# Optimization experiments

Measured on AMD Instinct MI355X. Metric: run time of the kernel, lower is better.

Reference implementation:

```python
import jax, jax.numpy as jnp
from jax import lax
import numpy as np

DN = ('NCDHW', 'OIDHW', 'NCDHW')
EPS = 1e-3  # BatchNorm1d eps=0.001
GRID = (41, 512, 512)  # spatial_shape [40,512,512] + [1,0,0]


def _block(x, mask, w, gamma, beta, rmean, rvar, stride, padding):
    # Regular (non-submanifold) sparse conv computes the same values as a dense
    # conv on the zero-filled grid; active OUTPUT sites are exactly those reached
    # by any active input site through the kernel window. BN+ReLU act only on
    # active sites (inactive sites stay exactly 0), hence the mask multiply.
    y = lax.conv_general_dilated(x, w, stride, padding, dimension_numbers=DN)
    k1 = jnp.ones((1, 1) + w.shape[2:], x.dtype)
    m = lax.conv_general_dilated(mask, k1, stride, padding, dimension_numbers=DN)
    m = (m > 0).astype(x.dtype)
    inv = gamma / jnp.sqrt(rvar + EPS)
    scale = inv.reshape(1, -1, 1, 1, 1)
    shift = (beta - rmean * inv).reshape(1, -1, 1, 1, 1)
    return jax.nn.relu(y * scale + shift) * m, m


def setup_inputs() -> dict:
    key = jax.random.key(0)
    NV, B = 120000, 2
    kf, kb, kz, ky, kx, kp = jax.random.split(key, 6)
    voxel_features = jax.random.normal(kf, (NV, 3), jnp.float32)
    coors = jnp.stack([
        jax.random.randint(kb, (NV,), 0, B, jnp.int32),
        jax.random.randint(kz, (NV,), 0, 40, jnp.int32),
        jax.random.randint(ky, (NV,), 0, 512, jnp.int32),
        jax.random.randint(kx, (NV,), 0, 512, jnp.int32)], axis=1)
    inp = {"voxel_features": voxel_features, "coors": coors, "batch_size": B}
    chans = [(3, 16, (3, 3, 3)), (16, 32, (3, 3, 3)), (32, 64, (3, 3, 3)), (64, 64, (3, 1, 1))]
    for i, (ci, co, k) in enumerate(chans, 1):
        kw, kg, kbb, km, kv = jax.random.split(jax.random.fold_in(kp, i), 5)
        fan = ci * k[0] * k[1] * k[2]
        inp[f"w{i}"] = jax.random.normal(kw, (co, ci) + k, jnp.float32) / np.sqrt(fan).astype(np.float32)
        inp[f"g{i}"] = jax.random.uniform(kg, (co,), jnp.float32, 0.5, 1.5)
        inp[f"bb{i}"] = jax.random.normal(kbb, (co,), jnp.float32) * 0.1
        inp[f"rm{i}"] = jax.random.normal(km, (co,), jnp.float32) * 0.1
        inp[f"rv{i}"] = jax.random.uniform(kv, (co,), jnp.float32, 0.5, 1.5)
    return inp


def reference(voxel_features, coors, batch_size,
              w1, g1, bb1, rm1, rv1,
              w2, g2, bb2, rm2, rv2,
              w3, g3, bb3, rm3, rv3,
              w4, g4, bb4, rm4, rv4):
    D, H, W = GRID
    C = voxel_features.shape[1]
    b, z, y, x = coors[:, 0], coors[:, 1], coors[:, 2], coors[:, 3]
    dense = jnp.zeros((batch_size, C, D, H, W), voxel_features.dtype)
    dense = dense.at[b, :, z, y, x].add(voxel_features)  # scatter voxels to grid
    mask = jnp.zeros((batch_size, 1, D, H, W), voxel_features.dtype).at[b, 0, z, y, x].set(1.0)
    h, m = _block(dense, mask, w1, g1, bb1, rm1, rv1, (2, 2, 2), [(1, 1), (1, 1), (1, 1)])
    h, m = _block(h, m, w2, g2, bb2, rm2, rv2, (2, 2, 2), [(1, 1), (1, 1), (1, 1)])
    h, m = _block(h, m, w3, g3, bb3, rm3, rv3, (2, 2, 2), [(0, 0), (1, 1), (1, 1)])
    h, m = _block(h, m, w4, g4, bb4, rm4, rv4, (2, 1, 1), [(0, 0), (0, 0), (0, 0)])
    N, Co, Dd, Hh, Ww = h.shape  # [B, 64, 2, 64, 64]
    return h.reshape(N, Co * Dd, Hh, Ww)
```

## Files before the change

kernel.cpp:

```cpp
#include <hip/hip_runtime.h>

#define EPS 1e-3f


static __device__ __forceinline__ unsigned f2bf(float f) {
    unsigned u = __float_as_uint(f);
    return (u + 0x7FFFu + ((u >> 16) & 1u)) >> 16;
}

typedef _Float16 f16x8 __attribute__((ext_vector_type(8)));
typedef float f32x4 __attribute__((ext_vector_type(4)));
typedef float f32x16 __attribute__((ext_vector_type(16)));

#define Y1_BYTES   88080384
#define SLACK_BYTE 2752512
#define SLACK_Y1   90832912

__global__ __launch_bounds__(256) void repack_prezero(
    const float* __restrict__ g1, const float* __restrict__ b1,
    const float* __restrict__ rm1, const float* __restrict__ rv1,
    const float* __restrict__ w2, const float* __restrict__ g2, const float* __restrict__ b2,
    const float* __restrict__ rm2, const float* __restrict__ rv2,
    const float* __restrict__ w3, const float* __restrict__ g3, const float* __restrict__ b3,
    const float* __restrict__ rm3, const float* __restrict__ rv3,
    const float* __restrict__ w4, const float* __restrict__ g4, const float* __restrict__ b4,
    const float* __restrict__ rm4, const float* __restrict__ rv4,
    _Float16* __restrict__ wB2, _Float16* __restrict__ wB3,
    _Float16* __restrict__ wB4, float* __restrict__ shb,
    const int* __restrict__ coors, int NV, unsigned short* __restrict__ y1,
    unsigned char* __restrict__ m1, float* __restrict__ m3)
{
    if (blockIdx.x >= 1034) {
        const int i = (blockIdx.x - 1034) * 256 + threadIdx.x;
        if (i < NV) {
            const int b = coors[4 * i + 0];
            const int z = coors[4 * i + 1];
            const int y = coors[4 * i + 2];
            const int x = coors[4 * i + 3];
            int ozv[2], nz = 0, oyv[2], ny = 0, oxv[2], nx = 0;
#pragma unroll
            for (int k = 0; k < 3; ++k) {
                int t = z + 1 - k;
                if (t >= 0 && !(t & 1)) { int o = t >> 1; if (o < 21) ozv[nz++] = o; }
            }
#pragma unroll
            for (int k = 0; k < 3; ++k) {
                int t = y + 1 - k;
                if (t >= 0 && !(t & 1)) { int o = t >> 1; if (o < 256) oyv[ny++] = o; }
            }
#pragma unroll
            for (int k = 0; k < 3; ++k) {
                int t = x + 1 - k;
                if (t >= 0 && !(t & 1)) { int o = t >> 1; if (o < 256) oxv[nx++] = o; }
            }
            const uint4 zz = {0u, 0u, 0u, 0u};
            for (int a = 0; a < nz; ++a)
                for (int bb = 0; bb < ny; ++bb)
                    for (int c = 0; c < nx; ++c) {
                        const int sp = ozv[a] * 65536 + oyv[bb] * 256 + oxv[c];
                        uint4* p = (uint4*)(y1 + (size_t)(b * 1376256 + sp) * 16);
                        p[0] = zz;
                        p[1] = zz;
                    }
        }
        asm volatile("s_waitcnt vmcnt(0)" ::: "memory");
        return;
    }
    if (blockIdx.x >= 321) {
        const int idx16 = (blockIdx.x - 321) * 256 + threadIdx.x;
        const uint4 zz = {0u, 0u, 0u, 0u};
        if (idx16 < 172034) {
            ((uint4*)m1)[idx16] = zz;
        } else if (idx16 < 182274) {
            ((uint4*)m3)[idx16 - 172034] = zz;
        }
        return;
    }

    const int i = blockIdx.x * 256 + threadIdx.x;
    if (i < 13824) {
        const int j = i & 7, lane = (i >> 3) & 63, tap = i >> 9;
        const int oc = lane & 31;
        const int cin = (lane >> 5) * 8 + j;
        const float inv = g2[oc] * rsqrtf(rv2[oc] + EPS);
        wB2[i] = (_Float16)(w2[(oc * 16 + cin) * 27 + tap] * inv);
    } else if (i >= 14336 && i < 69632) {
        const int j2 = i - 14336;
        const int j = j2 & 7, lane = (j2 >> 3) & 63, t = (j2 >> 9) & 3, tap = j2 >> 11;
        const int q = lane >> 4, n = lane & 15;
        const int oc = t * 16 + n;
        const int cin = q * 8 + j;
        const float inv = g3[oc] * rsqrtf(rv3[oc] + EPS);
        wB3[j2] = (_Float16)(w3[(oc * 32 + cin) * 27 + tap] * inv);
    } else if (i >= 69632 && i < 81920) {
        const int j2 = i - 69632;
        const int j = j2 & 7, lane = (j2 >> 3) & 63, t = (j2 >> 9) & 3, c = j2 >> 11;
        const int q = lane >> 4, n = lane & 15;
        const int oc = t * 16 + n;
        const int k = c * 32 + q * 8 + j;
        const int dz = k >> 6, cin = k & 63;
        const float inv = g4[oc] * rsqrtf(rv4[oc] + EPS);
        wB4[j2] = (_Float16)(w4[(oc * 64 + cin) * 3 + dz] * inv);
    } else if (i >= 81920 && i < 82112) {
        const int j = i - 81920;
        if (j < 32) {
            const float inv = g2[j] * rsqrtf(rv2[j] + EPS);
            shb[j] = b2[j] - rm2[j] * inv;
        } else if (j < 96) {
            const int o = j - 32;
            const float inv = g3[o] * rsqrtf(rv3[o] + EPS);
            shb[j] = b3[o] - rm3[o] * inv;
        } else if (j < 160) {
            const int o = j - 96;
            const float inv = g4[o] * rsqrtf(rv4[o] + EPS);
            shb[j] = b4[o] - rm4[o] * inv;
        } else if (j < 176) {
            const int o = j - 160;
            shb[j] = g1[o] * rsqrtf(rv1[o] + EPS);
        } else if (j < 192) {
            const int o = j - 176;
            const float inv = g1[o] * rsqrtf(rv1[o] + EPS);
            shb[j] = b1[o] - rm1[o] * inv;
        }
    }
}

__global__ __launch_bounds__(256) void scatter_l1(
    const float* __restrict__ vf, const int* __restrict__ coors, int NV,
    const float* __restrict__ w1, const float* __restrict__ shb,
    unsigned short* __restrict__ y1, unsigned char* __restrict__ m1)
{
    __shared__ float ws[16 * 3 * 27];
    for (int e = threadIdx.x; e < 16 * 3 * 27; e += 256)
        ws[e] = w1[e] * shb[160 + e / 81];
    __syncthreads();

    const int gid = blockIdx.x * 256 + threadIdx.x;
    const int i = gid >> 3;
    const int oc2 = gid & 7;
    if (i < NV) {
        const int oc = oc2 * 2;

        const int b = coors[4 * i + 0];
        const int z = coors[4 * i + 1];
        const int y = coors[4 * i + 2];
        const int x = coors[4 * i + 3];
        const float f0 = vf[3 * i + 0];
        const float f1 = vf[3 * i + 1];
        const float f2 = vf[3 * i + 2];

        int ozv[2], kzv[2], nz = 0;
        int oyv[2], kyv[2], ny = 0;
        int oxv[2], kxv[2], nx = 0;
#pragma unroll
        for (int k = 0; k < 3; ++k) {
            int t = z + 1 - k;
            if (t >= 0 && !(t & 1)) { int o = t >> 1; if (o < 21) { ozv[nz] = o; kzv[nz] = k; ++nz; } }
        }
#pragma unroll
        for (int k = 0; k < 3; ++k) {
            int t = y + 1 - k;
            if (t >= 0 && !(t & 1)) { int o = t >> 1; if (o < 256) { oyv[ny] = o; kyv[ny] = k; ++ny; } }
        }
#pragma unroll
        for (int k = 0; k < 3; ++k) {
            int t = x + 1 - k;
            if (t >= 0 && !(t & 1)) { int o = t >> 1; if (o < 256) { oxv[nx] = o; kxv[nx] = k; ++nx; } }
        }

        for (int a = 0; a < nz; ++a)
            for (int bb = 0; bb < ny; ++bb)
                for (int c = 0; c < nx; ++c) {
                    const int oz = ozv[a], oy = oyv[bb], ox = oxv[c];
                    const int tap = (kzv[a] * 3 + kyv[bb]) * 3 + kxv[c];
                    const int sp = oz * 65536 + oy * 256 + ox;
                    if (oc2 == 0) m1[b * 1376256 + sp] = 1;
                    const float s0 = ws[oc * 81 + tap] * f0 + ws[oc * 81 + 27 + tap] * f1 +
                                     ws[oc * 81 + 54 + tap] * f2;
                    const float s1 = ws[(oc + 1) * 81 + tap] * f0 +
                                     ws[(oc + 1) * 81 + 27 + tap] * f1 +
                                     ws[(oc + 1) * 81 + 54 + tap] * f2;
                    const unsigned pk = f2bf(s0) | (f2bf(s1) << 16);
                    unsigned* addr = (unsigned*)(y1 + (size_t)(b * 1376256 + sp) * 16 +
                                                 oc2 * 2);
                    asm volatile("global_atomic_pk_add_bf16 %0, %1, off"
                                 : : "v"(addr), "v"(pk) : "memory");
                }
    }
    asm volatile("s_waitcnt vmcnt(0)" ::: "memory");
}

__global__ __launch_bounds__(256) void masks_pass(
    const unsigned char* __restrict__ m1, float* __restrict__ m2,
    float* __restrict__ m3)
{
    const int idx = blockIdx.x * 256 + threadIdx.x;
    const int b = idx / 180224;
    const int r = idx - b * 180224;
    const int oz = r >> 14, r2 = r & 16383, oy = r2 >> 7, ox = r2 & 127;
    const int iz0 = 2 * oz - 1, iyb = 2 * oy - 1, ixb = 2 * ox - 1;
    unsigned msum = 0;
#pragma unroll
    for (int kz = 0; kz < 3; ++kz) {
        const int iz = iz0 + kz;
#pragma unroll
        for (int ky = 0; ky < 3; ++ky) {
            const int iy = iyb + ky;
#pragma unroll
            for (int kx = 0; kx < 3; ++kx) {
                const int ix = ixb + kx;
                if ((unsigned)iz < 21u && (unsigned)iy < 256u &&
                    (unsigned)ix < 256u)
                    msum |= m1[b * 1376256 + iz * 65536 + iy * 256 + ix];
            }
        }
    }
    m2[idx] = msum ? 1.f : 0.f;

    if (msum) {
        int ozv[2], nz = 0, oyv[2], ny = 0, oxv[2], nx = 0;
#pragma unroll
        for (int k = 0; k < 3; ++k) {
            int t = oz - k;
            if (t >= 0 && !(t & 1)) { int o = t >> 1; if (o < 5) ozv[nz++] = o; }
        }
#pragma unroll
        for (int k = 0; k < 3; ++k) {
            int t = oy + 1 - k;
            if (t >= 0 && !(t & 1)) { int o = t >> 1; if (o < 64) oyv[ny++] = o; }
        }
#pragma unroll
        for (int k = 0; k < 3; ++k) {
            int t = ox + 1 - k;
            if (t >= 0 && !(t & 1)) { int o = t >> 1; if (o < 64) oxv[nx++] = o; }
        }
        for (int a = 0; a < nz; ++a)
            for (int bb = 0; bb < ny; ++bb)
                for (int c = 0; c < nx; ++c)
                    m3[b * 20480 + ozv[a] * 4096 + oyv[bb] * 64 + oxv[c]] = 1.0f;
    }
}

__global__ __launch_bounds__(256) __attribute__((amdgpu_waves_per_eu(4, 8)))
void conv_l2(
    const unsigned char* __restrict__ y1c,
    const unsigned char* __restrict__ m1,
    const uint4* __restrict__ wB2,
    const float* __restrict__ m2, const float* __restrict__ shb,
    _Float16* __restrict__ h2h)
{
    const int tid = threadIdx.x;
    const int gw = blockIdx.x * 4 + (tid >> 6);
    const int lane = tid & 63;
    const int m = lane & 31, h = lane >> 5;

    const int plane = gw >> 9;
    const int rem = gw & 511;
    const int oy = rem >> 2;
    const int ox0 = (rem & 3) * 32;
    const int b = plane / 11, oz = plane % 11;
    const int iz0 = 2 * oz - 1, iyb = 2 * oy - 1;
    const int ixm = 2 * (ox0 + m) - 1;
    const int bbase = b * 1376256;
    const int qoff = h * 16;

    unsigned char mk[27];
#pragma unroll
    for (int t = 0; t < 27; ++t) {
        const int kz = t / 9, ky = (t / 3) % 3, kx = t % 3;
        const int iz = iz0 + kz, iy = iyb + ky, ix = ixm + kx;
        const bool v = (unsigned)iz < 21u && (unsigned)iy < 256u &&
                       (unsigned)ix < 256u;
        const int cell = bbase + iz * 65536 + iy * 256 + ix;
        mk[t] = m1[v ? cell : SLACK_BYTE];
    }

    float s1v[8];
    {
        const float4* sp = (const float4*)(shb + 176 + h * 8);
        const float4 a0 = sp[0], a1 = sp[1];
        s1v[0] = a0.x; s1v[1] = a0.y; s1v[2] = a0.z; s1v[3] = a0.w;
        s1v[4] = a1.x; s1v[5] = a1.y; s1v[6] = a1.z; s1v[7] = a1.w;
    }

    f32x16 acc;
#pragma unroll
    for (int r = 0; r < 16; ++r) acc[r] = 0.f;

    uint4 buf[13];
#pragma unroll
    for (int t = 0; t < 13; ++t) {
        const int kz = t / 9, ky = (t / 3) % 3, kx = t % 3;
        const int iz = iz0 + kz, iy = iyb + ky, ix = ixm + kx;
        const int cell = bbase + iz * 65536 + iy * 256 + ix;
        const int off = mk[t] ? (cell * 32 + qoff) : SLACK_Y1;
        buf[t] = *(const uint4*)(y1c + off);
    }

#pragma unroll
    for (int tap = 0; tap < 27; ++tap) {
        const int s = tap % 13;
        const uint4 ua = buf[s];
        const bool act = mk[s + (tap - s)] != 0;
        if (tap + 13 < 27) {
            const int t2 = tap + 13;
            const int kz = t2 / 9, ky = (t2 / 3) % 3, kx = t2 % 3;
            const int iz = iz0 + kz, iy = iyb + ky, ix = ixm + kx;
            const int cell = bbase + iz * 65536 + iy * 256 + ix;
            const int off = mk[t2] ? (cell * 32 + qoff) : SLACK_Y1;
            buf[s] = *(const uint4*)(y1c + off);
        }
        unsigned od[4];
        const unsigned dvs[4] = {ua.x, ua.y, ua.z, ua.w};
#pragma unroll
        for (int jj = 0; jj < 4; ++jj) {
            const unsigned dv = dvs[jj];
            const float vlo = fmaxf(__uint_as_float(dv << 16) + s1v[2 * jj], 0.f);
            const float vhi = fmaxf(__uint_as_float(dv & 0xFFFF0000u) + s1v[2 * jj + 1], 0.f);
            const unsigned pk =
                __builtin_bit_cast(unsigned, __builtin_amdgcn_cvt_pkrtz(vlo, vhi));
            od[jj] = act ? pk : 0u;
        }
        const uint4 uc = {od[0], od[1], od[2], od[3]};
        const f16x8 af = __builtin_bit_cast(f16x8, uc);
        const f16x8 bf = __builtin_bit_cast(f16x8, wB2[tap * 64 + lane]);
        acc = __builtin_amdgcn_mfma_f32_32x32x16_f16(af, bf, acc, 0, 0, 0);
    }

    const int oc = lane & 31;
#pragma unroll
    for (int r = 0; r < 16; ++r) {
        const int row = (r & 3) + 8 * (r >> 2) + 4 * h;
        const int px = ox0 + row;
        const int spo = oz * 16384 + oy * 128 + px;
        const float mv = m2[b * 180224 + spo];
        const size_t cbase = (size_t)(b * 180224 + spo) * 32;
        h2h[cbase + oc] = (_Float16)(fmaxf(acc[r] + shb[oc], 0.f) * mv);
    }
}

__global__ __launch_bounds__(256) __attribute__((amdgpu_waves_per_eu(4, 8)))
void conv_l3(
    const unsigned char* __restrict__ h2h,
    const uint4* __restrict__ wB3,
    const float* __restrict__ m3, const float* __restrict__ shb,
    _Float16* __restrict__ h3h)
{
    const int tid = threadIdx.x;
    const int gw = blockIdx.x * 4 + (tid >> 6);
    const int lane = tid & 63;
    const int m = lane & 15, q = lane >> 4;

    const int plane = gw >> 8;
    const int rem = gw & 255;
    const int oy = rem >> 2;
    const int ox0 = (rem & 3) * 16;
    const int b = plane / 5, oz = plane % 5;
    const int iz0 = 2 * oz, iyb = 2 * oy - 1;
    const int ixm = 2 * (ox0 + m) - 1;
    const int bbase = b * 180224;
    const int qoff = q * 16;

    f32x4 acc[4];
#pragma unroll
    for (int t = 0; t < 4; ++t) acc[t] = (f32x4){0.f, 0.f, 0.f, 0.f};

    uint4 buf[9];
    bool  val[9];
#pragma unroll
    for (int t = 0; t < 9; ++t) {
        const int ky = (t / 3) % 3, kx = t % 3;
        const int iz = iz0 + t / 9, iy = iyb + ky, ix = ixm + kx;
        const bool v = (unsigned)iy < 128u && (unsigned)ix < 128u;
        const int cell = bbase + iz * 16384 + iy * 128 + ix;
        buf[t] = *(const uint4*)(h2h + (v ? (cell * 64 + qoff) : 0));
        val[t] = v;
    }

#pragma unroll
    for (int tap = 0; tap < 27; ++tap) {
        const int s = tap % 9;
        uint4 ua = buf[s];
        if (!val[s]) { ua.x = 0; ua.y = 0; ua.z = 0; ua.w = 0; }
        if (tap + 9 < 27) {
            const int t2 = tap + 9;
            const int kz = t2 / 9, ky = (t2 / 3) % 3, kx = t2 % 3;
            const int iz = iz0 + kz, iy = iyb + ky, ix = ixm + kx;
            const bool v = (unsigned)iy < 128u && (unsigned)ix < 128u;
            const int cell = bbase + iz * 16384 + iy * 128 + ix;
            buf[s] = *(const uint4*)(h2h + (v ? (cell * 64 + qoff) : 0));
            val[s] = v;
        }
        const f16x8 af = __builtin_bit_cast(f16x8, ua);
#pragma unroll
        for (int t = 0; t < 4; ++t) {
            const f16x8 bf = __builtin_bit_cast(f16x8, wB3[(tap * 4 + t) * 64 + lane]);
            acc[t] = __builtin_amdgcn_mfma_f32_16x16x32_f16(af, bf, acc[t], 0, 0, 0);
        }
    }

    const int n = lane & 15;
#pragma unroll
    for (int r = 0; r < 4; ++r) {
        const int px = ox0 + q * 4 + r;
        const int spo = oz * 4096 + oy * 64 + px;
        const float mv = m3[b * 20480 + spo];
        const size_t cb = (size_t)(b * 20480 + spo) * 64;
#pragma unroll
        for (int t = 0; t < 4; ++t) {
            const int oc = t * 16 + n;
            h3h[cb + oc] = (_Float16)(fmaxf(acc[t][r] + shb[32 + oc], 0.f) * mv);
        }
    }
}

__global__ __launch_bounds__(256) __attribute__((amdgpu_waves_per_eu(4, 8)))
void conv_l4(
    const unsigned char* __restrict__ h3h,
    const uint4* __restrict__ wB4,
    const float* __restrict__ m3, const float* __restrict__ shb,
    float* __restrict__ out)
{
    const int tid = threadIdx.x;
    const int gw = blockIdx.x * 4 + (tid >> 6);
    const int lane = tid & 63;
    const int m = lane & 15, q = lane >> 4;

    const int b = gw >> 9, od = (gw >> 8) & 1;
    const int oy = (gw >> 2) & 63, ox0 = (gw & 3) * 16;
    const int cellbase = (b * 5 + 2 * od) * 4096 + oy * 64 + ox0 + m;

    f32x4 acc[4];
#pragma unroll
    for (int t = 0; t < 4; ++t) acc[t] = (f32x4){0.f, 0.f, 0.f, 0.f};

#pragma unroll
    for (int c = 0; c < 6; ++c) {
        const int dz = c >> 1;
        const size_t addr = (size_t)(cellbase + dz * 4096) * 128 +
                            (c & 1) * 64 + q * 16;
        const uint4 ua = *(const uint4*)(h3h + addr);
        const f16x8 af = __builtin_bit_cast(f16x8, ua);
#pragma unroll
        for (int t = 0; t < 4; ++t) {
            const f16x8 bf = __builtin_bit_cast(f16x8, wB4[(c * 4 + t) * 64 + lane]);
            acc[t] = __builtin_amdgcn_mfma_f32_16x16x32_f16(af, bf, acc[t], 0, 0, 0);
        }
    }

    const int n = lane & 15;
#pragma unroll
    for (int r = 0; r < 4; ++r) {
        const int px = ox0 + q * 4 + r;
        const int spo = oy * 64 + px;
        const float msum = m3[(b * 5 + 2 * od + 0) * 4096 + spo] +
                           m3[(b * 5 + 2 * od + 1) * 4096 + spo] +
                           m3[(b * 5 + 2 * od + 2) * 4096 + spo];
        const float mv = msum > 0.f ? 1.f : 0.f;
#pragma unroll
        for (int t = 0; t < 4; ++t) {
            const int oc = t * 16 + n;
            out[((b * 64 + oc) * 2 + od) * 4096 + spo] =
                fmaxf(acc[t][r] + shb[96 + oc], 0.f) * mv;
        }
    }
}

extern "C" void kernel_launch(void* const* d_in, const int* in_sizes, int n_in,
                              void* d_out, int out_size, void* d_ws, size_t ws_size,
                              hipStream_t stream)
{
    const float* vf    = (const float*)d_in[0];
    const int*   coors = (const int*)d_in[1];
    const float* w1 = (const float*)d_in[3];
    const float* g1 = (const float*)d_in[4];
    const float* b1 = (const float*)d_in[5];
    const float* rm1 = (const float*)d_in[6];
    const float* rv1 = (const float*)d_in[7];
    const float* w2 = (const float*)d_in[8];
    const float* g2 = (const float*)d_in[9];
    const float* b2 = (const float*)d_in[10];
    const float* rm2 = (const float*)d_in[11];
    const float* rv2 = (const float*)d_in[12];
    const float* w3 = (const float*)d_in[13];
    const float* g3 = (const float*)d_in[14];
    const float* b3 = (const float*)d_in[15];
    const float* rm3 = (const float*)d_in[16];
    const float* rv3 = (const float*)d_in[17];
    const float* w4 = (const float*)d_in[18];
    const float* g4 = (const float*)d_in[19];
    const float* b4 = (const float*)d_in[20];
    const float* rm4 = (const float*)d_in[21];
    const float* rv4 = (const float*)d_in[22];

    const int NV = in_sizes[0] / 3;

    float* ws = (float*)d_ws;
    float* y1  = ws;
    float* m1f = y1 + 22020096;
    float* h2h = m1f + 2752512;
    float* m2  = h2h + 5767168;
    float* h3h = m2 + 360448;
    float* m3  = h3h + 1310720;
    float* wB2 = m3 + 40960;
    float* wB3 = wB2 + 7168;
    float* wB4 = wB3 + 27648;
    float* shb = wB4 + 6144;

    unsigned char* m1 = (unsigned char*)m1f;

    const int pzBlocks = (NV + 255) / 256;
    repack_prezero<<<1034 + pzBlocks, 256, 0, stream>>>(
        g1, b1, rm1, rv1,
        w2, g2, b2, rm2, rv2, w3, g3, b3, rm3, rv3,
        w4, g4, b4, rm4, rv4,
        (_Float16*)wB2, (_Float16*)wB3, (_Float16*)wB4, shb,
        coors, NV, (unsigned short*)y1, m1, m3);
    scatter_l1<<<(NV * 8 + 255) / 256, 256, 0, stream>>>(vf, coors, NV, w1, shb,
                                                         (unsigned short*)y1, m1);
    masks_pass<<<1408, 256, 0, stream>>>(m1, m2, m3);
    conv_l2<<<2816, 256, 0, stream>>>((const unsigned char*)d_ws, m1,
                                      (const uint4*)wB2, m2, shb, (_Float16*)h2h);
    conv_l3<<<640, 256, 0, stream>>>((const unsigned char*)h2h, (const uint4*)wB3,
                                     m3, shb, (_Float16*)h3h);
    conv_l4<<<256, 256, 0, stream>>>((const unsigned char*)h3h, (const uint4*)wB4,
                                     m3, shb, (float*)d_out);
}
```

Measured before the change: 201.7 us.

## Stage conv_l2 input rows in LDS via global_load_lds with swizzle

The layer-2 conv kernel now has each block cover a full output row (4 waves × 32 x-positions). For each kz slice it cooperatively loads the three needed input rows into swizzled shared memory using direct global-to-LDS loads. Taps then read from LDS instead of issuing per-tap gathered global loads, so overlapping stride-2 windows reuse the same data and memory requests get more coalesced. Block indices are also remapped to interleave planes, and the per-tap mask is packed into a bitfield. The cost is added barriers per kz slice, no overlap between loading and compute, and 25 KB of LDS per block that may limit occupancy.

Measured after the change: 202.4 us. Within noise of the previous version (+0.4%).

```diff
diff --git a/kernel.cpp b/kernel.cpp
--- a/kernel.cpp
+++ b/kernel.cpp
@@ -12,7 +12,6 @@
 typedef float f32x4 __attribute__((ext_vector_type(4)));
 typedef float f32x16 __attribute__((ext_vector_type(16)));
 
-#define Y1_BYTES   88080384
 #define SLACK_BYTE 2752512
 #define SLACK_Y1   90832912
 
@@ -249,22 +248,25 @@
     const float* __restrict__ m2, const float* __restrict__ shb,
     _Float16* __restrict__ h2h)
 {
+    __shared__ unsigned char lds[3 * 8320];
+
     const int tid = threadIdx.x;
-    const int gw = blockIdx.x * 4 + (tid >> 6);
     const int lane = tid & 63;
+    const int w = tid >> 6;
     const int m = lane & 31, h = lane >> 5;
 
-    const int plane = gw >> 9;
-    const int rem = gw & 511;
-    const int oy = rem >> 2;
-    const int ox0 = (rem & 3) * 32;
-    const int b = plane / 11, oz = plane % 11;
+    const int sbid = (blockIdx.x & 7) * 352 + (blockIdx.x >> 3);
+    const int oy = sbid / 22;
+    const int plane = sbid - oy * 22;
+    const int b = plane / 11, oz = plane - b * 11;
+
+    const int ox0 = w * 32;
     const int iz0 = 2 * oz - 1, iyb = 2 * oy - 1;
     const int ixm = 2 * (ox0 + m) - 1;
     const int bbase = b * 1376256;
     const int qoff = h * 16;
 
-    unsigned char mk[27];
+    unsigned mbits = 0;
 #pragma unroll
     for (int t = 0; t < 27; ++t) {
         const int kz = t / 9, ky = (t / 3) % 3, kx = t % 3;
@@ -272,7 +274,7 @@
         const bool v = (unsigned)iz < 21u && (unsigned)iy < 256u &&
                        (unsigned)ix < 256u;
         const int cell = bbase + iz * 65536 + iy * 256 + ix;
-        mk[t] = m1[v ? cell : SLACK_BYTE];
+        mbits |= (unsigned)(m1[v ? cell : SLACK_BYTE] & 1) << t;
     }
 
     float s1v[8];
@@ -283,48 +285,81 @@
         s1v[4] = a1.x; s1v[5] = a1.y; s1v[6] = a1.z; s1v[7] = a1.w;
     }
 
+    int rdo[3];
+#pragma unroll
+    for (int kx = 0; kx < 3; ++kx) {
+        const unsigned lx = (unsigned)(2 * (ox0 + m) + kx);
+        const unsigned L = lx * 32 + qoff;
+        rdo[kx] = (int)(L ^ (((L >> 7) & 7u) << 4));
+    }
+
+    int su_row[7], su_ix[7], su_half[7];
+#pragma unroll
+    for (int it = 0; it < 7; ++it) {
+        const int t = it * 256 + tid;
+        const int row = t / 520;
+        const int u = t - row * 520;
+        const unsigned L = (unsigned)(u * 16) ^ (((unsigned)(u >> 3) & 7u) << 4);
+        su_row[it] = row;
+        su_ix[it] = (int)(L >> 5) - 1;
+        su_half[it] = (int)((L >> 4) & 1u);
+    }
+
     f32x16 acc;
 #pragma unroll
     for (int r = 0; r < 16; ++r) acc[r] = 0.f;
 
-    uint4 buf[13];
-#pragma unroll
-    for (int t = 0; t < 13; ++t) {
-        const int kz = t / 9, ky = (t / 3) % 3, kx = t % 3;
-        const int iz = iz0 + kz, iy = iyb + ky, ix = ixm + kx;
-        const int cell = bbase + iz * 65536 + iy * 256 + ix;
-        const int off = mk[t] ? (cell * 32 + qoff) : SLACK_Y1;
-        buf[t] = *(const uint4*)(y1c + off);
-    }
-
-#pragma unroll
-    for (int tap = 0; tap < 27; ++tap) {
-        const int s = tap % 13;
-        const uint4 ua = buf[s];
-        const bool act = mk[s + (tap - s)] != 0;
-        if (tap + 13 < 27) {
-            const int t2 = tap + 13;
-            const int kz = t2 / 9, ky = (t2 / 3) % 3, kx = t2 % 3;
-            const int iz = iz0 + kz, iy = iyb + ky, ix = ixm + kx;
-            const int cell = bbase + iz * 65536 + iy * 256 + ix;
-            const int off = mk[t2] ? (cell * 32 + qoff) : SLACK_Y1;
-            buf[s] = *(const uint4*)(y1c + off);
-        }
-        unsigned od[4];
-        const unsigned dvs[4] = {ua.x, ua.y, ua.z, ua.w};
-#pragma unroll
-        for (int jj = 0; jj < 4; ++jj) {
-            const unsigned dv = dvs[jj];
-            const float vlo = fmaxf(__uint_as_float(dv << 16) + s1v[2 * jj], 0.f);
-            const float vhi = fmaxf(__uint_as_float(dv & 0xFFFF0000u) + s1v[2 * jj + 1], 0.f);
-            const unsigned pk =
-                __builtin_bit_cast(unsigned, __builtin_amdgcn_cvt_pkrtz(vlo, vhi));
-            od[jj] = act ? pk : 0u;
-        }
-        const uint4 uc = {od[0], od[1], od[2], od[3]};
-        const f16x8 af = __builtin_bit_cast(f16x8, uc);
-        const f16x8 bf = __builtin_bit_cast(f16x8, wB2[tap * 64 + lane]);
-        acc = __builtin_amdgcn_mfma_f32_32x32x16_f16(af, bf, acc, 0, 0, 0);
+    for (int kz = 0; kz < 3; ++kz) {
+        const int iz = iz0 + kz;
+        const bool izok = (unsigned)iz < 21u;
+        const int zrow = bbase + iz * 65536;
+
+        __syncthreads();
+#pragma unroll
+        for (int it = 0; it < 7; ++it) {
+            const int t = it * 256 + tid;
+            if (t < 1560) {
+                const int row = su_row[it];
+                const int iy = iyb + row;
+                const int ix = su_ix[it];
+                const bool v = izok && (unsigned)iy < 256u && (unsigned)ix < 256u;
+                const int srcb = v ? ((zrow + iy * 256 + ix) * 32 + su_half[it] * 16)
+                                   : (int)SLACK_Y1;
+                const int bt = t - lane;
+                __builtin_amdgcn_global_load_lds(
+                    (const __attribute__((address_space(1))) unsigned char*)(y1c + srcb),
+                    (__attribute__((address_space(3))) unsigned char*)(lds + bt * 16),
+                    16, 0, 0);
+            }
+        }
+        asm volatile("s_waitcnt vmcnt(0)" ::: "memory");
+        __syncthreads();
+
+#pragma unroll
+        for (int ky = 0; ky < 3; ++ky) {
+            const int rbase = ky * 8320;
+#pragma unroll
+            for (int kx = 0; kx < 3; ++kx) {
+                const int tap = kz * 9 + ky * 3 + kx;
+                const uint4 ua = *(const uint4*)(lds + rbase + rdo[kx]);
+                const bool act = (mbits >> tap) & 1u;
+                unsigned od[4];
+                const unsigned dvs[4] = {ua.x, ua.y, ua.z, ua.w};
+#pragma unroll
+                for (int jj = 0; jj < 4; ++jj) {
+                    const unsigned dv = dvs[jj];
+                    const float vlo = fmaxf(__uint_as_float(dv << 16) + s1v[2 * jj], 0.f);
+                    const float vhi = fmaxf(__uint_as_float(dv & 0xFFFF0000u) + s1v[2 * jj + 1], 0.f);
+                    const unsigned pk = __builtin_bit_cast(
+                        unsigned, __builtin_amdgcn_cvt_pkrtz(vlo, vhi));
+                    od[jj] = act ? pk : 0u;
+                }
+                const uint4 uc = {od[0], od[1], od[2], od[3]};
+                const f16x8 af = __builtin_bit_cast(f16x8, uc);
+                const f16x8 bf = __builtin_bit_cast(f16x8, wB2[tap * 64 + lane]);
+                acc = __builtin_amdgcn_mfma_f32_32x32x16_f16(af, bf, acc, 0, 0, 0);
+            }
+        }
     }
 
     const int oc = lane & 31;
```
